# Kernel optimization log

Hardware: AMD Instinct MI355X
Metric: run time of the kernel (lower is better)

Reference implementation:

```python
import jax, jax.numpy as jnp
import numpy as np
from jax import lax

DIM = 64
HEADS = 4
B, Q, V = 8, 128, 128


def _modrelu(z, b):
    m = jnp.abs(z)
    return z * (jax.nn.relu(m + b) / (m + 1e-5))


def _eunn_unitary(h, th1, ph1, th2, ph2, om):
    # tunable-style EUNN, capacity 2: even-pair rotations, odd-pair rotations, diagonal phase
    d = h.shape[-1]
    # layer 1: pairs (0,1),(2,3),...
    hp = h.reshape(*h.shape[:-1], d // 2, 2)
    a, b = hp[..., 0], hp[..., 1]
    c1, s1, e1 = jnp.cos(th1), jnp.sin(th1), jnp.exp(1j * ph1)
    h = jnp.stack([e1 * (c1 * a - s1 * b), s1 * a + c1 * b], -1).reshape(h.shape)
    # layer 2: pairs (1,2),(3,4),...,(d-3,d-2); endpoints pass through
    mid = h[..., 1:d - 1].reshape(*h.shape[:-1], d // 2 - 1, 2)
    a, b = mid[..., 0], mid[..., 1]
    c2, s2, e2 = jnp.cos(th2), jnp.sin(th2), jnp.exp(1j * ph2)
    mid2 = jnp.stack([e2 * (c2 * a - s2 * b), s2 * a + c2 * b], -1).reshape(*h.shape[:-1], d - 2)
    h = jnp.concatenate([h[..., :1], mid2, h[..., d - 1:]], -1)
    return h * jnp.exp(1j * om)


def _forward(queries, values, U_re, U_im, bias, theta1, phi1, theta2, phi2, omega, W_dense, b_dense):
    Bq, Qq, d = queries.shape
    Vv = values.shape[1]
    # quadratic (query, value) expansion -> [B*Q, V, 2d]
    dq = jnp.broadcast_to(queries[:, :, None, :], (Bq, Qq, Vv, d))
    dv = jnp.broadcast_to(values[:, None, :, :], (Bq, Qq, Vv, d))
    x = jnp.concatenate([dq, dv], -1).reshape(Bq * Qq, Vv, 2 * d)
    U = (U_re + 1j * U_im)  # [H, 2d, d] complex input kernel per head
    Ux = jnp.einsum('nvi,hij->hvnj', x.astype(jnp.complex64), U)  # [H, V, N, d]

    def run_head(Ux_h, t1, p1, t2, p2, om, bh):
        def step(h, u):
            h2 = _modrelu(_eunn_unitary(h, t1, p1, t2, p2, om) + u, bh)
            return h2, None
        h0 = jnp.zeros(Ux_h.shape[1:], dtype=jnp.complex64)  # [N, d]
        hT, _ = lax.scan(step, h0, Ux_h)
        return hT  # final state, as Keras RNN with return_sequences=False

    outs = jax.vmap(run_head)(Ux, theta1, phi1, theta2, phi2, omega, bias)  # [H, N, d]
    acc = jnp.real(outs).transpose(1, 0, 2).reshape(Bq * Qq, HEADS * d)
    y = acc @ W_dense + b_dense
    return y.reshape(Bq, Qq, d)


def setup_inputs() -> dict:
    key = jax.random.key(0)
    ks = jax.random.split(key, 12)
    pi = np.pi
    return {
        'queries': jax.random.normal(ks[0], (B, Q, DIM), jnp.float32),
        'values': jax.random.normal(ks[1], (B, V, DIM), jnp.float32),
        'U_re': jax.random.normal(ks[2], (HEADS, 2 * DIM, DIM), jnp.float32) * (1.0 / np.sqrt(2 * DIM)),
        'U_im': jax.random.normal(ks[3], (HEADS, 2 * DIM, DIM), jnp.float32) * (1.0 / np.sqrt(2 * DIM)),
        'bias': jax.random.normal(ks[4], (HEADS, DIM), jnp.float32) * 0.01,
        'theta1': jax.random.uniform(ks[5], (HEADS, DIM // 2), jnp.float32, -pi, pi),
        'phi1': jax.random.uniform(ks[6], (HEADS, DIM // 2), jnp.float32, -pi, pi),
        'theta2': jax.random.uniform(ks[7], (HEADS, DIM // 2 - 1), jnp.float32, -pi, pi),
        'phi2': jax.random.uniform(ks[8], (HEADS, DIM // 2 - 1), jnp.float32, -pi, pi),
        'omega': jax.random.uniform(ks[9], (HEADS, DIM), jnp.float32, -pi, pi),
        'W_dense': jax.random.normal(ks[10], (HEADS * DIM, DIM), jnp.float32) * (1.0 / np.sqrt(HEADS * DIM)),
        'b_dense': jnp.zeros((DIM,), jnp.float32),
    }


def reference(queries, values, U_re, U_im, bias, theta1, phi1, theta2, phi2, omega, W_dense, b_dense):
    return _forward(queries, values, U_re, U_im, bias, theta1, phi1, theta2, phi2, omega, W_dense, b_dense)
```

## Files before the change

### kernel.cpp

```cpp
#include <hip/hip_runtime.h>
#include <math.h>

#define DIM 64
#define HEADS 4
#define BB 8
#define QQ 128
#define VV 128
#define NN (BB*QQ)

typedef float f2 __attribute__((ext_vector_type(2)));

__device__ __forceinline__ float dpp_swap1(float x) {
    return __int_as_float(__builtin_amdgcn_update_dpp(
        0, __float_as_int(x), 0xB1, 0xF, 0xF, true));
}
__device__ __forceinline__ float dpp_wshr1(float x) {
    return __int_as_float(__builtin_amdgcn_update_dpp(
        0, __float_as_int(x), 0x138, 0xF, 0xF, true));
}
__device__ __forceinline__ float dpp_wshl1(float x) {
    return __int_as_float(__builtin_amdgcn_update_dpp(
        0, __float_as_int(x), 0x130, 0xF, 0xF, true));
}
__device__ __forceinline__ f2 dpp2_swap1(f2 x) {
    f2 r; r.x = dpp_swap1(x.x); r.y = dpp_swap1(x.y); return r;
}
__device__ __forceinline__ f2 dpp2_shl1(f2 x) {
    f2 r; r.x = dpp_wshl1(x.x); r.y = dpp_wshl1(x.y); return r;
}
__device__ __forceinline__ f2 dpp2_shr1(f2 x) {
    f2 r; r.x = dpp_wshr1(x.x); r.y = dpp_wshr1(x.y); return r;
}

#define GLOAD(dst, ptr, OFFSTR) \
    asm volatile("global_load_dwordx2 %0, %1, off offset:" OFFSTR \
                 : "=v"(dst) : "v"(ptr))

__global__ __launch_bounds__(256) void k_av(const float* __restrict__ values,
                                            const float* __restrict__ U_re,
                                            const float* __restrict__ U_im,
                                            f2* __restrict__ Av) {
    int tid = blockIdx.x * blockDim.x + threadIdx.x;
    int w = tid >> 6;
    int j = tid & 63;
    int h = w >> 9;
    int r0 = (w & 511) << 1;
    const float* vrow = values + r0 * DIM;
    const float* ur = U_re + (h * 2 * DIM + DIM) * DIM + j;
    const float* ui = U_im + (h * 2 * DIM + DIM) * DIM + j;
    f2 a0 = 0.f, a1 = 0.f;
    #pragma unroll 8
    for (int i = 0; i < DIM; ++i) {
        f2 u; u.x = ur[i * DIM]; u.y = ui[i * DIM];
        a0 += vrow[i] * u;
        a1 += vrow[DIM + i] * u;
    }
    f2* out = Av + (h * 1024 + r0) * DIM + j;
    out[0] = a0; out[DIM] = a1;
}

__global__ __launch_bounds__(256) void k_rnn_dense(
        const float* __restrict__ queries,
        const float* __restrict__ U_re,
        const float* __restrict__ U_im,
        const float* __restrict__ bias,
        const float* __restrict__ theta1,
        const float* __restrict__ phi1,
        const float* __restrict__ theta2,
        const float* __restrict__ phi2,
        const float* __restrict__ omega,
        const f2* __restrict__ Av,
        const float* __restrict__ W_dense,
        const float* __restrict__ b_dense,
        float* __restrict__ y) {
    int b = blockIdx.x >> 6;
    int q = blockIdx.x & 63;
    int t = threadIdx.x;
    int h = t >> 6;
    int j = t & 63;
    int n0 = b * 128 + q;
    int n1 = n0 + 64;

    int k1 = j >> 1;
    float th1 = theta1[h * 32 + k1], ph1 = phi1[h * 32 + k1];
    float C1 = cosf(th1);
    float s1v = sinf(th1);
    float S1, E1r, E1i;
    if ((j & 1) == 0) {
        S1 = -s1v; E1r = cosf(ph1); E1i = sinf(ph1);
    } else {
        S1 = s1v; E1r = 1.f; E1i = 0.f;
    }

    float C2, SL, SR, p2r, p2i;
    if (j == 0 || j == 63) {
        C2 = 1.f; SL = 0.f; SR = 0.f; p2r = 1.f; p2i = 0.f;
    } else {
        int k2 = (j - 1) >> 1;
        float th2 = theta2[h * 31 + k2], ph2 = phi2[h * 31 + k2];
        float c2 = cosf(th2), s2 = sinf(th2);
        if (j & 1) {
            C2 = c2; SL = -s2; SR = 0.f;
            p2r = cosf(ph2); p2i = sinf(ph2);
        } else {
            C2 = c2; SR = s2; SL = 0.f;
            p2r = 1.f; p2i = 0.f;
        }
    }
    float om = omega[h * 64 + j];
    float eor = cosf(om), eoi = sinf(om);
    float PHr = p2r * eor - p2i * eoi;
    float PHi = p2r * eoi + p2i * eor;

    float bj = bias[h * 64 + j];

    const float* qrow0 = queries + n0 * DIM;
    const float* qrow1 = queries + n1 * DIM;
    const float* ur = U_re + (h * 2 * DIM) * DIM + j;
    const float* ui = U_im + (h * 2 * DIM) * DIM + j;
    f2 Uqr = 0.f, Uqi = 0.f;
    #pragma unroll 8
    for (int i = 0; i < DIM; ++i) {
        f2 a; a.x = qrow0[i]; a.y = qrow1[i];
        float wr = ur[i * DIM], wi = ui[i * DIM];
        Uqr += a * wr;
        Uqi += a * wi;
    }

    f2 Hr = 0.f, Hi = 0.f;
    auto step = [&](f2 av) {
        f2 uvr = Uqr + av.x;
        f2 uvi = Uqi + av.y;
        f2 Pr = dpp2_swap1(Hr), Pi = dpp2_swap1(Hi);
        f2 tpr = C1 * Hr + S1 * Pr;
        f2 tpi = C1 * Hi + S1 * Pi;
        f2 Tr = E1r * tpr - E1i * tpi;
        f2 Ti = E1r * tpi + E1i * tpr;
        f2 Lr = dpp2_shl1(Tr), Li = dpp2_shl1(Ti);
        f2 Rr = dpp2_shr1(Tr), Ri = dpp2_shr1(Ti);
        f2 spr = C2 * Tr + SL * Lr + SR * Rr;
        f2 spi = C2 * Ti + SL * Li + SR * Ri;
        f2 Zr = (PHr * spr - PHi * spi) + uvr;
        f2 Zi = (PHr * spi + PHi * spr) + uvi;
        f2 q2 = Zr * Zr + Zi * Zi + 1e-10f;
        float rsx = __builtin_amdgcn_rsqf(q2.x);
        float rsy = __builtin_amdgcn_rsqf(q2.y);
        f2 sc;
        sc.x = fmaxf(fmaf(bj, rsx, 1.f), 0.f);
        sc.y = fmaxf(fmaf(bj, rsy, 1.f), 0.f);
        Hr = Zr * sc; Hi = Zi * sc;
    };

    const f2* pcur = Av + (h * 1024 + b * 128) * DIM + j;

    f2 c0, c1, c2v, c3, c4, c5, c6, c7;
    GLOAD(c0, pcur, "0");    GLOAD(c1, pcur, "512");
    GLOAD(c2v, pcur, "1024"); GLOAD(c3, pcur, "1536");
    GLOAD(c4, pcur, "2048"); GLOAD(c5, pcur, "2560");
    GLOAD(c6, pcur, "3072"); GLOAD(c7, pcur, "3584");
    asm volatile("s_waitcnt vmcnt(0)"
                 : "+v"(c0), "+v"(c1), "+v"(c2v), "+v"(c3),
                   "+v"(c4), "+v"(c5), "+v"(c6), "+v"(c7));

    for (int vb = 0; vb < VV; vb += 8) {
        const f2* pn = (vb < VV - 8) ? (pcur + 8 * DIM) : pcur;
        f2 x0, x1, x2, x3, x4, x5, x6, x7;
        GLOAD(x0, pn, "0");    GLOAD(x1, pn, "512");
        GLOAD(x2, pn, "1024"); GLOAD(x3, pn, "1536");
        GLOAD(x4, pn, "2048"); GLOAD(x5, pn, "2560");
        GLOAD(x6, pn, "3072"); GLOAD(x7, pn, "3584");
        step(c0); step(c1); step(c2v); step(c3);
        step(c4); step(c5); step(c6); step(c7);
        asm volatile("s_waitcnt vmcnt(0)"
                     : "+v"(x0), "+v"(x1), "+v"(x2), "+v"(x3),
                       "+v"(x4), "+v"(x5), "+v"(x6), "+v"(x7));
        c0 = x0; c1 = x1; c2v = x2; c3 = x3;
        c4 = x4; c5 = x5; c6 = x6; c7 = x7;
        pcur = pn;
    }

    __shared__ float s_acc[2][HEADS * DIM];
    __shared__ float s_part[256];
    s_acc[0][h * 64 + j] = Hr.x;
    s_acc[1][h * 64 + j] = Hr.y;
    __syncthreads();

    {
        int r = t >> 7, hf = (t >> 6) & 1, jj = t & 63;
        const float* Wp = W_dense + (hf * 128) * DIM + jj;
        const float* ap = &s_acc[r][hf * 128];
        float part = 0.f;
        #pragma unroll 8
        for (int k = 0; k < 128; ++k)
            part = fmaf(ap[k], Wp[k * DIM], part);
        s_part[t] = part;
    }
    __syncthreads();
    if (t < 128) {
        int r = t >> 6, jj = t & 63;
        y[(n0 + r * 64) * DIM + jj] =
            b_dense[jj] + s_part[r * 128 + jj] + s_part[r * 128 + 64 + jj];
    }
}

extern "C" void kernel_launch(void* const* d_in, const int* in_sizes, int n_in,
                              void* d_out, int out_size, void* d_ws, size_t ws_size,
                              hipStream_t stream) {
    const float* queries = (const float*)d_in[0];
    const float* values  = (const float*)d_in[1];
    const float* U_re    = (const float*)d_in[2];
    const float* U_im    = (const float*)d_in[3];
    const float* bias    = (const float*)d_in[4];
    const float* theta1  = (const float*)d_in[5];
    const float* phi1    = (const float*)d_in[6];
    const float* theta2  = (const float*)d_in[7];
    const float* phi2    = (const float*)d_in[8];
    const float* omega   = (const float*)d_in[9];
    const float* W_dense = (const float*)d_in[10];
    const float* b_dense = (const float*)d_in[11];
    float* y = (float*)d_out;

    f2* Av = (f2*)d_ws;

    k_av<<<512, 256, 0, stream>>>(values, U_re, U_im, Av);
    k_rnn_dense<<<512, 256, 0, stream>>>(queries, U_re, U_im, bias, theta1,
                                         phi1, theta2, phi2, omega, Av,
                                         W_dense, b_dense, y);
}
```

Baseline: 116.3 us.

## Process four query rows per thread in the RNN kernel, halving the grid

Each thread now carries four independent recurrent states (query rows spaced 32 apart) instead of two, so each loaded Av value and each DPP permutation setup serves more work, and the grid drops from 512 to 256 blocks. The dense epilogue is simplified so each thread computes one full output over all 256 inputs, which removes the second shared-memory reduction stage. More work per thread raises ILP to hide latency along the serial recurrence, at the cost of more registers and only 256 blocks to spread over the GPU's compute units.

```diff
diff --git a/kernel.cpp b/kernel.cpp
--- a/kernel.cpp
+++ b/kernel.cpp
@@ -9,28 +9,23 @@
 #define NN (BB*QQ)
 
 typedef float f2 __attribute__((ext_vector_type(2)));
-
-__device__ __forceinline__ float dpp_swap1(float x) {
+typedef float f4 __attribute__((ext_vector_type(4)));
+
+template <int CTRL>
+__device__ __forceinline__ float dppf(float x) {
     return __int_as_float(__builtin_amdgcn_update_dpp(
-        0, __float_as_int(x), 0xB1, 0xF, 0xF, true));
-}
-__device__ __forceinline__ float dpp_wshr1(float x) {
-    return __int_as_float(__builtin_amdgcn_update_dpp(
-        0, __float_as_int(x), 0x138, 0xF, 0xF, true));
-}
-__device__ __forceinline__ float dpp_wshl1(float x) {
-    return __int_as_float(__builtin_amdgcn_update_dpp(
-        0, __float_as_int(x), 0x130, 0xF, 0xF, true));
-}
-__device__ __forceinline__ f2 dpp2_swap1(f2 x) {
-    f2 r; r.x = dpp_swap1(x.x); r.y = dpp_swap1(x.y); return r;
-}
-__device__ __forceinline__ f2 dpp2_shl1(f2 x) {
-    f2 r; r.x = dpp_wshl1(x.x); r.y = dpp_wshl1(x.y); return r;
-}
-__device__ __forceinline__ f2 dpp2_shr1(f2 x) {
-    f2 r; r.x = dpp_wshr1(x.x); r.y = dpp_wshr1(x.y); return r;
-}
+        0, __float_as_int(x), CTRL, 0xF, 0xF, true));
+}
+template <int CTRL>
+__device__ __forceinline__ f4 dpp4(f4 x) {
+    f4 r;
+    r.x = dppf<CTRL>(x.x); r.y = dppf<CTRL>(x.y);
+    r.z = dppf<CTRL>(x.z); r.w = dppf<CTRL>(x.w);
+    return r;
+}
+#define SWAP1 0xB1
+#define WSHR1 0x138
+#define WSHL1 0x130
 
 #define GLOAD(dst, ptr, OFFSTR) \
     asm volatile("global_load_dwordx2 %0, %1, off offset:" OFFSTR \
@@ -59,7 +54,7 @@
     out[0] = a0; out[DIM] = a1;
 }
 
-__global__ __launch_bounds__(256) void k_rnn_dense(
+__global__ __launch_bounds__(256, 1) void k_rnn_dense(
         const float* __restrict__ queries,
         const float* __restrict__ U_re,
         const float* __restrict__ U_im,
@@ -73,24 +68,18 @@
         const float* __restrict__ W_dense,
         const float* __restrict__ b_dense,
         float* __restrict__ y) {
-    int b = blockIdx.x >> 6;
-    int q = blockIdx.x & 63;
+    int b = blockIdx.x >> 5;
+    int q0 = blockIdx.x & 31;
     int t = threadIdx.x;
     int h = t >> 6;
     int j = t & 63;
-    int n0 = b * 128 + q;
-    int n1 = n0 + 64;
 
     int k1 = j >> 1;
     float th1 = theta1[h * 32 + k1], ph1 = phi1[h * 32 + k1];
-    float C1 = cosf(th1);
-    float s1v = sinf(th1);
+    float C1 = cosf(th1), s1v = sinf(th1);
     float S1, E1r, E1i;
-    if ((j & 1) == 0) {
-        S1 = -s1v; E1r = cosf(ph1); E1i = sinf(ph1);
-    } else {
-        S1 = s1v; E1r = 1.f; E1i = 0.f;
-    }
+    if ((j & 1) == 0) { S1 = -s1v; E1r = cosf(ph1); E1i = sinf(ph1); }
+    else              { S1 =  s1v; E1r = 1.f;       E1i = 0.f;       }
 
     float C2, SL, SR, p2r, p2i;
     if (j == 0 || j == 63) {
@@ -99,55 +88,56 @@
         int k2 = (j - 1) >> 1;
         float th2 = theta2[h * 31 + k2], ph2 = phi2[h * 31 + k2];
         float c2 = cosf(th2), s2 = sinf(th2);
-        if (j & 1) {
-            C2 = c2; SL = -s2; SR = 0.f;
-            p2r = cosf(ph2); p2i = sinf(ph2);
-        } else {
-            C2 = c2; SR = s2; SL = 0.f;
-            p2r = 1.f; p2i = 0.f;
-        }
+        if (j & 1) { C2 = c2; SL = -s2; SR = 0.f; p2r = cosf(ph2); p2i = sinf(ph2); }
+        else       { C2 = c2; SR =  s2; SL = 0.f; p2r = 1.f;       p2i = 0.f;       }
     }
     float om = omega[h * 64 + j];
     float eor = cosf(om), eoi = sinf(om);
     float PHr = p2r * eor - p2i * eoi;
     float PHi = p2r * eoi + p2i * eor;
-
     float bj = bias[h * 64 + j];
 
-    const float* qrow0 = queries + n0 * DIM;
-    const float* qrow1 = queries + n1 * DIM;
+    int nbase = b * 128 + q0;
+    const float* qrow0 = queries + (nbase      ) * DIM;
+    const float* qrow1 = queries + (nbase + 32 ) * DIM;
+    const float* qrow2 = queries + (nbase + 64 ) * DIM;
+    const float* qrow3 = queries + (nbase + 96 ) * DIM;
     const float* ur = U_re + (h * 2 * DIM) * DIM + j;
     const float* ui = U_im + (h * 2 * DIM) * DIM + j;
-    f2 Uqr = 0.f, Uqi = 0.f;
+    f4 Uqr = 0.f, Uqi = 0.f;
     #pragma unroll 8
     for (int i = 0; i < DIM; ++i) {
-        f2 a; a.x = qrow0[i]; a.y = qrow1[i];
+        f4 a; a.x = qrow0[i]; a.y = qrow1[i]; a.z = qrow2[i]; a.w = qrow3[i];
         float wr = ur[i * DIM], wi = ui[i * DIM];
         Uqr += a * wr;
         Uqi += a * wi;
     }
 
-    f2 Hr = 0.f, Hi = 0.f;
+    f4 Hr = 0.f, Hi = 0.f;
     auto step = [&](f2 av) {
-        f2 uvr = Uqr + av.x;
-        f2 uvi = Uqi + av.y;
-        f2 Pr = dpp2_swap1(Hr), Pi = dpp2_swap1(Hi);
-        f2 tpr = C1 * Hr + S1 * Pr;
-        f2 tpi = C1 * Hi + S1 * Pi;
-        f2 Tr = E1r * tpr - E1i * tpi;
-        f2 Ti = E1r * tpi + E1i * tpr;
-        f2 Lr = dpp2_shl1(Tr), Li = dpp2_shl1(Ti);
-        f2 Rr = dpp2_shr1(Tr), Ri = dpp2_shr1(Ti);
-        f2 spr = C2 * Tr + SL * Lr + SR * Rr;
-        f2 spi = C2 * Ti + SL * Li + SR * Ri;
-        f2 Zr = (PHr * spr - PHi * spi) + uvr;
-        f2 Zi = (PHr * spi + PHi * spr) + uvi;
-        f2 q2 = Zr * Zr + Zi * Zi + 1e-10f;
-        float rsx = __builtin_amdgcn_rsqf(q2.x);
-        float rsy = __builtin_amdgcn_rsqf(q2.y);
-        f2 sc;
-        sc.x = fmaxf(fmaf(bj, rsx, 1.f), 0.f);
-        sc.y = fmaxf(fmaf(bj, rsy, 1.f), 0.f);
+        f4 uvr = Uqr + av.x;
+        f4 uvi = Uqi + av.y;
+        f4 Pr = dpp4<SWAP1>(Hr), Pi = dpp4<SWAP1>(Hi);
+        f4 tpr = C1 * Hr + S1 * Pr;
+        f4 tpi = C1 * Hi + S1 * Pi;
+        f4 Tr = E1r * tpr - E1i * tpi;
+        f4 Ti = E1r * tpi + E1i * tpr;
+        f4 Lr = dpp4<WSHL1>(Tr), Li = dpp4<WSHL1>(Ti);
+        f4 Rr = dpp4<WSHR1>(Tr), Ri = dpp4<WSHR1>(Ti);
+        f4 spr = C2 * Tr + SL * Lr + SR * Rr;
+        f4 spi = C2 * Ti + SL * Li + SR * Ri;
+        f4 Zr = (PHr * spr - PHi * spi) + uvr;
+        f4 Zi = (PHr * spi + PHi * spr) + uvi;
+        f4 q2;
+        q2.x = fmaf(Zr.x, Zr.x, fmaf(Zi.x, Zi.x, 1e-10f));
+        q2.y = fmaf(Zr.y, Zr.y, fmaf(Zi.y, Zi.y, 1e-10f));
+        q2.z = fmaf(Zr.z, Zr.z, fmaf(Zi.z, Zi.z, 1e-10f));
+        q2.w = fmaf(Zr.w, Zr.w, fmaf(Zi.w, Zi.w, 1e-10f));
+        f4 sc;
+        sc.x = fmaxf(fmaf(bj, __builtin_amdgcn_rsqf(q2.x), 1.f), 0.f);
+        sc.y = fmaxf(fmaf(bj, __builtin_amdgcn_rsqf(q2.y), 1.f), 0.f);
+        sc.z = fmaxf(fmaf(bj, __builtin_amdgcn_rsqf(q2.z), 1.f), 0.f);
+        sc.w = fmaxf(fmaf(bj, __builtin_amdgcn_rsqf(q2.w), 1.f), 0.f);
         Hr = Zr * sc; Hi = Zi * sc;
     };
 
@@ -179,27 +169,22 @@
         pcur = pn;
     }
 
-    __shared__ float s_acc[2][HEADS * DIM];
-    __shared__ float s_part[256];
+    __shared__ float s_acc[4][HEADS * DIM];
     s_acc[0][h * 64 + j] = Hr.x;
     s_acc[1][h * 64 + j] = Hr.y;
+    s_acc[2][h * 64 + j] = Hr.z;
+    s_acc[3][h * 64 + j] = Hr.w;
     __syncthreads();
 
     {
-        int r = t >> 7, hf = (t >> 6) & 1, jj = t & 63;
-        const float* Wp = W_dense + (hf * 128) * DIM + jj;
-        const float* ap = &s_acc[r][hf * 128];
-        float part = 0.f;
+        int r = t >> 6, jj = t & 63;
+        const float* ap = s_acc[r];
+        const float* Wp = W_dense + jj;
+        float acc = b_dense[jj];
         #pragma unroll 8
-        for (int k = 0; k < 128; ++k)
-            part = fmaf(ap[k], Wp[k * DIM], part);
-        s_part[t] = part;
-    }
-    __syncthreads();
-    if (t < 128) {
-        int r = t >> 6, jj = t & 63;
-        y[(n0 + r * 64) * DIM + jj] =
-            b_dense[jj] + s_part[r * 128 + jj] + s_part[r * 128 + 64 + jj];
+        for (int k = 0; k < HEADS * DIM; ++k)
+            acc = fmaf(ap[k], Wp[k * DIM], acc);
+        y[(nbase + 32 * r) * DIM + jj] = acc;
     }
 }
 
@@ -223,7 +208,7 @@
     f2* Av = (f2*)d_ws;
 
     k_av<<<512, 256, 0, stream>>>(values, U_re, U_im, Av);
-    k_rnn_dense<<<512, 256, 0, stream>>>(queries, U_re, U_im, bias, theta1,
+    k_rnn_dense<<<256, 256, 0, stream>>>(queries, U_re, U_im, bias, theta1,
                                          phi1, theta2, phi2, omega, Av,
                                          W_dense, b_dense, y);
 }
```

After: 123.8 us. +6.4%, slower.
